# Performance work log

Hardware: AMD Instinct MI355X
Metric: run time of the kernel (lower is better)

The kernel has to match this reference:

```python
import jax, jax.numpy as jnp
import numpy as np

ALPHA = 0.2  # LeakyReLU negative slope


def setup_inputs() -> dict:
    key = jax.random.key(0)
    k1, k2, k3 = jax.random.split(key, 3)
    B, N, D_in, D_out = 16, 2048, 128, 128
    x = jax.random.normal(k1, (B, N, D_in), dtype=jnp.float32)
    # xavier-uniform-ish scale for params
    W = jax.random.normal(k2, (D_in, D_out), dtype=jnp.float32) * (1.414 / np.sqrt(D_in + D_out))
    a = jax.random.normal(k3, (2 * D_out, 1), dtype=jnp.float32) * (1.414 / np.sqrt(2 * D_out + 1))
    return {"x": x, "W": W, "a": a}


def reference(x, W, a):
    # h: (B, N, D)
    h = jnp.matmul(x, W)
    D = h.shape[-1]
    # a = [a1; a2]; e[b,i,j] = leakyrelu(a1 . h_i + a2 . h_j)
    a1 = a[:D, 0]   # (D,)
    a2 = a[D:, 0]   # (D,)
    s1 = jnp.einsum('bnd,d->bn', h, a1)  # (B, N) source term
    s2 = jnp.einsum('bnd,d->bn', h, a2)  # (B, N) target term
    e = jax.nn.leaky_relu(s1[:, :, None] + s2[:, None, :], negative_slope=ALPHA)  # (B, N, N)
    attention = jax.nn.softmax(e, axis=2)
    h_prime = jnp.matmul(attention, h)  # (B, N, D)
    return jax.nn.relu(h_prime)  # concat=True -> relu
```

## Files before the change

### kernel.cpp

```cpp
#include <hip/hip_runtime.h>
#include <hip/hip_bf16.h>
#include <cstddef>

#define GAT_B 16
#define GAT_N 2048
#define GAT_D 128
#define GAT_ROWS (GAT_B * GAT_N)
#define CH 128
#define CL 16
#define GAT_ALPHA 0.2f

typedef __attribute__((ext_vector_type(8))) short short8v;
typedef __attribute__((ext_vector_type(4))) float f32x4;

__device__ __forceinline__ void cvt_hilo(float x, unsigned short& hi, unsigned short& lo) {
  union { float f; unsigned u; } a;
  a.f = x;
  hi = (unsigned short)(a.u >> 16);
  union { unsigned u; float f; } b;
  b.u = (unsigned)hi << 16;
  union { float f; unsigned u; } c;
  c.f = x - b.f;
  lo = (unsigned short)(c.u >> 16);
}

__global__ __launch_bounds__(256) void k0_wfrag(const float* __restrict__ W,
                                                unsigned short* __restrict__ WfH,
                                                unsigned short* __restrict__ WfL) {
  const int t = blockIdx.x * 256 + threadIdx.x;
  const int n = t & 127, g = (t >> 7) & 3, ks = t >> 9;
  short8v vh, vl;
#pragma unroll
  for (int j = 0; j < 8; ++j) {
    const int k = ks * 32 + g * 8 + j;
    unsigned short hi, lo;
    cvt_hilo(W[k * 128 + n], hi, lo);
    vh[j] = (short)hi;
    vl[j] = (short)lo;
  }
  *(short8v*)&WfH[t * 8] = vh;
  *(short8v*)&WfL[t * 8] = vl;
}

__global__ __launch_bounds__(256) void k1_gemm(const float* __restrict__ x,
                                               const unsigned short* __restrict__ WfHg,
                                               const unsigned short* __restrict__ WfLg,
                                               const float* __restrict__ aa,
                                               float* __restrict__ h,
                                               float* __restrict__ s1part,
                                               float* __restrict__ s2part) {
  __shared__ unsigned short xH[64 * 128];
  __shared__ unsigned short xL[64 * 128];
  const int tid = threadIdx.x;
  const int row0 = blockIdx.x * 64;

#pragma unroll
  for (int p = 0; p < 8; ++p) {
    const int row = p * 8 + (tid >> 5);
    const int f4 = tid & 31;
    const float4 v = ((const float4*)(x + (size_t)(row0 + row) * GAT_D))[f4];
    unsigned short h0, h1, h2, h3, l0, l1, l2, l3;
    cvt_hilo(v.x, h0, l0);
    cvt_hilo(v.y, h1, l1);
    cvt_hilo(v.z, h2, l2);
    cvt_hilo(v.w, h3, l3);
    const int slot = (f4 >> 1) ^ (row & 7);
    const int base = row * 128 + slot * 8 + (f4 & 1) * 4;
    *(ushort4*)&xH[base] = make_ushort4(h0, h1, h2, h3);
    *(ushort4*)&xL[base] = make_ushort4(l0, l1, l2, l3);
  }

  const int w = tid >> 6, l = tid & 63;
  const int wc0 = w * 32;
  const int g = l >> 4, c16 = l & 15;

  short8v bh[4][2], bl[4][2];
#pragma unroll
  for (int ks = 0; ks < 4; ++ks)
#pragma unroll
    for (int nt = 0; nt < 2; ++nt) {
      const int bi = ((ks * 4 + g) * 128 + wc0 + nt * 16 + c16) * 8;
      bh[ks][nt] = *(const short8v*)&WfHg[bi];
      bl[ks][nt] = *(const short8v*)&WfLg[bi];
    }

  __syncthreads();

  f32x4 acc[4][2];
#pragma unroll
  for (int mt = 0; mt < 4; ++mt)
#pragma unroll
    for (int nt = 0; nt < 2; ++nt) acc[mt][nt] = (f32x4)(0.f);

#pragma unroll
  for (int ks = 0; ks < 4; ++ks) {
    short8v ah[4], al[4];
#pragma unroll
    for (int mt = 0; mt < 4; ++mt) {
      const int row = mt * 16 + c16;
      const int ai = row * 128 + (((ks * 4 + g) ^ (row & 7)) * 8);
      ah[mt] = *(const short8v*)&xH[ai];
      al[mt] = *(const short8v*)&xL[ai];
    }
#pragma unroll
    for (int mt = 0; mt < 4; ++mt) {
#pragma unroll
      for (int nt = 0; nt < 2; ++nt) {
        acc[mt][nt] = __builtin_amdgcn_mfma_f32_16x16x32_bf16(ah[mt], bh[ks][nt], acc[mt][nt], 0, 0, 0);
        acc[mt][nt] = __builtin_amdgcn_mfma_f32_16x16x32_bf16(al[mt], bh[ks][nt], acc[mt][nt], 0, 0, 0);
        acc[mt][nt] = __builtin_amdgcn_mfma_f32_16x16x32_bf16(ah[mt], bl[ks][nt], acc[mt][nt], 0, 0, 0);
      }
    }
  }

#pragma unroll
  for (int mt = 0; mt < 4; ++mt)
#pragma unroll
    for (int nt = 0; nt < 2; ++nt)
#pragma unroll
      for (int j = 0; j < 4; ++j)
        h[(size_t)(row0 + mt * 16 + g * 4 + j) * GAT_D + wc0 + nt * 16 + c16] =
            acc[mt][nt][j];

  float a1v[2], a2v[2];
#pragma unroll
  for (int nt = 0; nt < 2; ++nt) {
    a1v[nt] = aa[wc0 + nt * 16 + c16];
    a2v[nt] = aa[128 + wc0 + nt * 16 + c16];
  }
#pragma unroll
  for (int mt = 0; mt < 4; ++mt) {
#pragma unroll
    for (int j = 0; j < 4; ++j) {
      float t1 = acc[mt][0][j] * a1v[0] + acc[mt][1][j] * a1v[1];
      float t2 = acc[mt][0][j] * a2v[0] + acc[mt][1][j] * a2v[1];
#pragma unroll
      for (int off = 1; off < 16; off <<= 1) {
        t1 += __shfl_xor(t1, off);
        t2 += __shfl_xor(t2, off);
      }
      if (c16 == 0) {
        const int row = row0 + mt * 16 + g * 4 + j;
        s1part[w * GAT_ROWS + row] = t1;
        s2part[w * GAT_ROWS + row] = t2;
      }
    }
  }
}

__global__ __launch_bounds__(1024) void k2_sort(const float* __restrict__ s1part,
                                                const float* __restrict__ s2part,
                                                float* __restrict__ s2s,
                                                int* __restrict__ idxs,
                                                float* __restrict__ s1s,
                                                int* __restrict__ rids,
                                                float* __restrict__ wA,
                                                float* __restrict__ wP,
                                                float* __restrict__ preDenA,
                                                float* __restrict__ sufDenP) {
  __shared__ float v[2048];
  __shared__ int id[2048];
  __shared__ float wtotA[16];
  __shared__ float wtotP[16];
  const int tid = threadIdx.x;
  const int b = blockIdx.x >> 1;
  const int half = blockIdx.x & 1;
  const int i0 = tid, i1 = tid + 1024;
  const float* src = (half == 0) ? s2part : s1part;
  {
    const int r0 = b * GAT_N + i0, r1 = b * GAT_N + i1;
    float v0 = src[r0] + src[GAT_ROWS + r0] + src[2 * GAT_ROWS + r0] + src[3 * GAT_ROWS + r0];
    float v1 = src[r1] + src[GAT_ROWS + r1] + src[2 * GAT_ROWS + r1] + src[3 * GAT_ROWS + r1];
    if (half == 1) {
      v0 = -v0;
      v1 = -v1;
    }
    v[i0] = v0;
    v[i1] = v1;
  }
  id[i0] = i0;
  id[i1] = i1;
  for (int k = 2; k <= 2048; k <<= 1) {
    for (int j = k >> 1; j > 0; j >>= 1) {
      __syncthreads();
      const int i = ((tid & ~(j - 1)) << 1) | (tid & (j - 1));
      const int ixj = i | j;
      const bool up = (i & k) == 0;
      const float va = v[i], vb = v[ixj];
      if (up ? (va > vb) : (va < vb)) {
        v[i] = vb;
        v[ixj] = va;
        const int ta = id[i];
        id[i] = id[ixj];
        id[ixj] = ta;
      }
    }
  }
  __syncthreads();
  if (half == 1) {
    s1s[b * GAT_N + i0] = -v[i0];
    s1s[b * GAT_N + i1] = -v[i1];
    rids[b * GAT_N + i0] = id[i0];
    rids[b * GAT_N + i1] = id[i1];
    return;
  }
  s2s[b * GAT_N + i0] = v[i0];
  s2s[b * GAT_N + i1] = v[i1];
  idxs[b * GAT_N + i0] = id[i0];
  idxs[b * GAT_N + i1] = id[i1];

  const int lane = tid & 63, w = tid >> 6;
  const float aL = __expf(GAT_ALPHA * v[2 * tid]);
  const float aR = __expf(GAT_ALPHA * v[2 * tid + 1]);
  const float pL = __expf(v[2047 - 2 * tid]);
  const float pR = __expf(v[2046 - 2 * tid]);
  wA[b * GAT_N + 2 * tid] = aL;
  wA[b * GAT_N + 2 * tid + 1] = aR;
  wP[b * GAT_N + 2047 - 2 * tid] = pL;
  wP[b * GAT_N + 2046 - 2 * tid] = pR;
  float sA = aL + aR, sP = pL + pR;
#pragma unroll
  for (int off = 1; off < 64; off <<= 1) {
    const float tA = __shfl_up(sA, off);
    const float tP = __shfl_up(sP, off);
    if (lane >= off) {
      sA += tA;
      sP += tP;
    }
  }
  if (lane == 63) {
    wtotA[w] = sA;
    wtotP[w] = sP;
  }
  __syncthreads();
  float offA = 0.f, offP = 0.f;
  for (int ww = 0; ww < w; ++ww) {
    offA += wtotA[ww];
    offP += wtotP[ww];
  }
  const float inclA = offA + sA;
  const float inclP = offP + sP;
  preDenA[b * GAT_N + 2 * tid] = inclA - aR;
  preDenA[b * GAT_N + 2 * tid + 1] = inclA;
  sufDenP[b * GAT_N + 2047 - 2 * tid] = inclP - pR;
  sufDenP[b * GAT_N + 2046 - 2 * tid] = inclP;
}

__global__ __launch_bounds__(128) void k3_permute(const float* __restrict__ h,
                                                  const int* __restrict__ idxs,
                                                  const float* __restrict__ wA,
                                                  const float* __restrict__ wP,
                                                  float* __restrict__ hs,
                                                  float* __restrict__ partA,
                                                  float* __restrict__ partP) {
  const int b = blockIdx.x >> 7, c = blockIdx.x & (CH - 1);
  const int d = threadIdx.x;
  const int q0 = c * CL;
  const int* idxb = idxs + b * GAT_N;
  const float* hb = h + (size_t)b * GAT_N * GAT_D;
  float accA = 0.f, accP = 0.f;
#pragma unroll
  for (int qq = 0; qq < CL; ++qq) {
    const int q = q0 + qq;
    const int j = idxb[q];
    const float hv = hb[(size_t)j * GAT_D + d];
    hs[((size_t)b * GAT_N + q) * GAT_D + d] = hv;
    accA = fmaf(wA[b * GAT_N + q], hv, accA);
    accP = fmaf(wP[b * GAT_N + q], hv, accP);
  }
  partA[(b * CH + c) * GAT_D + d] = accA;
  partP[(b * CH + c) * GAT_D + d] = accP;
}

__global__ __launch_bounds__(1024) void k3b_prep(const float* __restrict__ s1s,
                                                 const float* __restrict__ s2s,
                                                 const float* __restrict__ preDenA,
                                                 const float* __restrict__ sufDenP,
                                                 const float* __restrict__ partA,
                                                 const float* __restrict__ partP,
                                                 float* __restrict__ baseA,
                                                 float* __restrict__ baseP,
                                                 int* __restrict__ pArr,
                                                 float* __restrict__ c1,
                                                 float* __restrict__ c2) {
  __shared__ float totA[8][128];
  __shared__ float totP[8][128];
  __shared__ float sh[2048];
  const int b = blockIdx.x >> 1;
  const int role = blockIdx.x & 1;
  const int t = threadIdx.x;
  if (role == 0) {
    const int d = t & 127, g = t >> 7;
    const float* pA = partA + (size_t)(b * CH + g * 16) * GAT_D + d;
    const float* pP = partP + (size_t)(b * CH + g * 16) * GAT_D + d;
    float la[16], lp[16];
    float sA = 0.f, sP = 0.f;
#pragma unroll
    for (int i = 0; i < 16; ++i) {
      la[i] = pA[i * GAT_D];
      sA += la[i];
      lp[i] = pP[i * GAT_D];
      sP += lp[i];
    }
    totA[g][d] = sA;
    totP[g][d] = sP;
    __syncthreads();
    float offA = 0.f, offP = 0.f;
    for (int gg = 0; gg < g; ++gg) offA += totA[gg][d];
    for (int gg = g + 1; gg < 8; ++gg) offP += totP[gg][d];
    float run = offA;
#pragma unroll
    for (int i = 0; i < 16; ++i) {
      baseA[(size_t)(b * (CH + 1) + g * 16 + i) * GAT_D + d] = run;
      run += la[i];
    }
    if (g == 7) baseA[(size_t)(b * (CH + 1) + CH) * GAT_D + d] = run;
    run = offP;
#pragma unroll
    for (int i = 15; i >= 0; --i) {
      baseP[(size_t)(b * CH + g * 16 + i) * GAT_D + d] = run;
      run += lp[i];
    }
  } else {
    sh[t] = s2s[b * GAT_N + t];
    sh[t + 1024] = s2s[b * GAT_N + t + 1024];
    __syncthreads();
#pragma unroll
    for (int rr = 0; rr < 2; ++rr) {
      const int j = t + rr * 1024;
      const float s1v = s1s[b * GAT_N + j];
      const float tt = -s1v;
      int lo = 0, hi = GAT_N;
      while (lo < hi) {
        const int mid = (lo + hi) >> 1;
        if (sh[mid] < tt)
          lo = mid + 1;
        else
          hi = mid;
      }
      const float e1 = __expf(s1v), e2 = __expf(GAT_ALPHA * s1v);
      float den = 0.f;
      if (lo < GAT_N) den += e1 * sufDenP[b * GAT_N + lo];
      if (lo > 0) den += e2 * preDenA[b * GAT_N + lo - 1];
      const float inv = 1.f / den;
      pArr[b * GAT_N + j] = lo;
      c1[b * GAT_N + j] = e1 * inv;
      c2[b * GAT_N + j] = e2 * inv;
    }
  }
}

__global__ __launch_bounds__(256) void k5_out(const float* __restrict__ hs,
                                              const float* __restrict__ wA,
                                              const float* __restrict__ wP,
                                              const float* __restrict__ baseA,
                                              const float* __restrict__ baseP,
                                              const int* __restrict__ pArr,
                                              const float* __restrict__ c1,
                                              const float* __restrict__ c2,
                                              const int* __restrict__ rids,
                                              float* __restrict__ out) {
  const int wave = threadIdx.x >> 6, lane = threadIdx.x & 63;
  const int j = blockIdx.x * 4 + wave;
  const int b = j >> 11;
  const int jr = b * GAT_N + (j & 2047);
  const int p = pArr[jr];
  const float cc1 = c1[jr], cc2 = c2[jr];
  const int rid = rids[jr];
  const float2* hs2 = (const float2*)(hs + (size_t)b * GAT_N * GAT_D);
  const float* wAb = wA + b * GAT_N;
  const float* wPb = wP + b * GAT_N;

  const int cA = p >> 4;
  float2 accA = ((const float2*)(baseA + (size_t)(b * (CH + 1) + cA) * GAT_D))[lane];
  for (int q = cA * CL; q < p; ++q) {
    const float w = wAb[q];
    const float2 hv = hs2[(size_t)q * 64 + lane];
    accA.x = fmaf(w, hv.x, accA.x);
    accA.y = fmaf(w, hv.y, accA.y);
  }

  const int pP = p < GAT_N ? p : GAT_N - 1;
  const int cP = pP >> 4;
  float2 accP = ((const float2*)(baseP + (size_t)(b * CH + cP) * GAT_D))[lane];
  const int qend = cP * CL + CL;
  for (int q = p; q < qend; ++q) {
    const float w = wPb[q];
    const float2 hv = hs2[(size_t)q * 64 + lane];
    accP.x = fmaf(w, hv.x, accP.x);
    accP.y = fmaf(w, hv.y, accP.y);
  }

  const float vx = cc2 * accA.x + cc1 * accP.x;
  const float vy = cc2 * accA.y + cc1 * accP.y;
  ((float2*)out)[(size_t)(b * GAT_N + rid) * 64 + lane] =
      make_float2(fmaxf(vx, 0.f), fmaxf(vy, 0.f));
}

extern "C" void kernel_launch(void* const* d_in, const int* in_sizes, int n_in,
                              void* d_out, int out_size, void* d_ws, size_t ws_size,
                              hipStream_t stream) {
  (void)in_sizes;
  (void)n_in;
  (void)out_size;
  (void)ws_size;
  const float* x = (const float*)d_in[0];
  const float* W = (const float*)d_in[1];
  const float* a = (const float*)d_in[2];
  float* out = (float*)d_out;
  float* wsf = (float*)d_ws;

  const size_t HN = (size_t)GAT_ROWS * GAT_D;
  size_t o = 0;
  float* s1part = wsf + o;   o += 4 * GAT_ROWS;
  float* s2part = wsf + o;   o += 4 * GAT_ROWS;
  float* s2s = wsf + o;      o += GAT_ROWS;
  int* idxs = (int*)(wsf + o); o += GAT_ROWS;
  float* s1s = wsf + o;      o += GAT_ROWS;
  int* rids = (int*)(wsf + o); o += GAT_ROWS;
  float* preDenA = wsf + o;  o += GAT_ROWS;
  float* sufDenP = wsf + o;  o += GAT_ROWS;
  float* wAr = wsf + o;      o += GAT_ROWS;
  float* wPr = wsf + o;      o += GAT_ROWS;
  int* pArr = (int*)(wsf + o); o += GAT_ROWS;
  float* c1 = wsf + o;       o += GAT_ROWS;
  float* c2 = wsf + o;       o += GAT_ROWS;
  float* partA = wsf + o;    o += (size_t)GAT_B * CH * GAT_D;
  float* partP = wsf + o;    o += (size_t)GAT_B * CH * GAT_D;
  float* baseA = wsf + o;    o += (size_t)GAT_B * (CH + 1) * GAT_D;
  float* baseP = wsf + o;    o += (size_t)GAT_B * CH * GAT_D;
  unsigned short* WfH = (unsigned short*)(wsf + o); o += 8192;
  unsigned short* WfL = (unsigned short*)(wsf + o); o += 8192;
  float* h = wsf + o;        o += HN;
  float* hs = wsf + o;       o += HN;

  k0_wfrag<<<8, 256, 0, stream>>>(W, WfH, WfL);
  k1_gemm<<<512, 256, 0, stream>>>(x, WfH, WfL, a, h, s1part, s2part);
  k2_sort<<<2 * GAT_B, 1024, 0, stream>>>(s1part, s2part, s2s, idxs, s1s, rids, wAr, wPr,
                                          preDenA, sufDenP);
  k3_permute<<<GAT_B * CH, 128, 0, stream>>>(h, idxs, wAr, wPr, hs, partA, partP);
  k3b_prep<<<2 * GAT_B, 1024, 0, stream>>>(s1s, s2s, preDenA, sufDenP, partA, partP,
                                           baseA, baseP, pArr, c1, c2);
  k5_out<<<GAT_ROWS / 4, 256, 0, stream>>>(hs, wAr, wPr, baseA, baseP, pArr, c1, c2,
                                           rids, out);
}
```

Before: 82.05 us.

## Replace bitonic sort with parallel rank sort and drop permuted h copy

Replaces the 32-block bitonic sort with a 256-block rank-by-counting kernel using packed 64-bit keys, so each element's sorted position comes from comparing against all 2048 keys in shared memory. The prefix sums of the exp weights move into k3b_prep's shared memory instead of global arrays. The materialized permuted copy hs is removed, and k3 and k5 now gather h through idxs. Chunk size is halved (CL 8, CH 256) to shorten the per-row tail loops. This trades the sort's many barrier phases for O(N) comparisons per element and indirect gathers in the output kernel.

```diff
diff --git a/kernel.cpp b/kernel.cpp
--- a/kernel.cpp
+++ b/kernel.cpp
@@ -6,8 +6,8 @@
 #define GAT_N 2048
 #define GAT_D 128
 #define GAT_ROWS (GAT_B * GAT_N)
-#define CH 128
-#define CL 16
+#define CH 256
+#define CL 8
 #define GAT_ALPHA 0.2f
 
 typedef __attribute__((ext_vector_type(8))) short short8v;
@@ -148,112 +148,59 @@
   }
 }
 
-__global__ __launch_bounds__(1024) void k2_sort(const float* __restrict__ s1part,
+__global__ __launch_bounds__(256) void k2a_rank(const float* __restrict__ s1part,
                                                 const float* __restrict__ s2part,
                                                 float* __restrict__ s2s,
                                                 int* __restrict__ idxs,
                                                 float* __restrict__ s1s,
                                                 int* __restrict__ rids,
                                                 float* __restrict__ wA,
-                                                float* __restrict__ wP,
-                                                float* __restrict__ preDenA,
-                                                float* __restrict__ sufDenP) {
-  __shared__ float v[2048];
-  __shared__ int id[2048];
-  __shared__ float wtotA[16];
-  __shared__ float wtotP[16];
-  const int tid = threadIdx.x;
-  const int b = blockIdx.x >> 1;
-  const int half = blockIdx.x & 1;
-  const int i0 = tid, i1 = tid + 1024;
-  const float* src = (half == 0) ? s2part : s1part;
-  {
-    const int r0 = b * GAT_N + i0, r1 = b * GAT_N + i1;
-    float v0 = src[r0] + src[GAT_ROWS + r0] + src[2 * GAT_ROWS + r0] + src[3 * GAT_ROWS + r0];
-    float v1 = src[r1] + src[GAT_ROWS + r1] + src[2 * GAT_ROWS + r1] + src[3 * GAT_ROWS + r1];
-    if (half == 1) {
-      v0 = -v0;
-      v1 = -v1;
-    }
-    v[i0] = v0;
-    v[i1] = v1;
-  }
-  id[i0] = i0;
-  id[i1] = i1;
-  for (int k = 2; k <= 2048; k <<= 1) {
-    for (int j = k >> 1; j > 0; j >>= 1) {
-      __syncthreads();
-      const int i = ((tid & ~(j - 1)) << 1) | (tid & (j - 1));
-      const int ixj = i | j;
-      const bool up = (i & k) == 0;
-      const float va = v[i], vb = v[ixj];
-      if (up ? (va > vb) : (va < vb)) {
-        v[i] = vb;
-        v[ixj] = va;
-        const int ta = id[i];
-        id[i] = id[ixj];
-        id[ixj] = ta;
-      }
-    }
+                                                float* __restrict__ wP) {
+  __shared__ unsigned long long keys[2048];
+  const int blk = blockIdx.x;
+  const int b = blk >> 4;
+  const int key = (blk >> 3) & 1;
+  const int chunk = blk & 7;
+  const int t = threadIdx.x;
+  const float* src = key ? s1part : s2part;
+#pragma unroll
+  for (int ii = 0; ii < 8; ++ii) {
+    const int i = t + ii * 256;
+    const int r = b * GAT_N + i;
+    float v = src[r] + src[GAT_ROWS + r] + src[2 * GAT_ROWS + r] + src[3 * GAT_ROWS + r];
+    if (key) v = -v;
+    unsigned u = __float_as_uint(v);
+    u = (u & 0x80000000u) ? ~u : (u | 0x80000000u);
+    keys[i] = ((unsigned long long)u << 11) | (unsigned)i;
   }
   __syncthreads();
-  if (half == 1) {
-    s1s[b * GAT_N + i0] = -v[i0];
-    s1s[b * GAT_N + i1] = -v[i1];
-    rids[b * GAT_N + i0] = id[i0];
-    rids[b * GAT_N + i1] = id[i1];
-    return;
-  }
-  s2s[b * GAT_N + i0] = v[i0];
-  s2s[b * GAT_N + i1] = v[i1];
-  idxs[b * GAT_N + i0] = id[i0];
-  idxs[b * GAT_N + i1] = id[i1];
-
-  const int lane = tid & 63, w = tid >> 6;
-  const float aL = __expf(GAT_ALPHA * v[2 * tid]);
-  const float aR = __expf(GAT_ALPHA * v[2 * tid + 1]);
-  const float pL = __expf(v[2047 - 2 * tid]);
-  const float pR = __expf(v[2046 - 2 * tid]);
-  wA[b * GAT_N + 2 * tid] = aL;
-  wA[b * GAT_N + 2 * tid + 1] = aR;
-  wP[b * GAT_N + 2047 - 2 * tid] = pL;
-  wP[b * GAT_N + 2046 - 2 * tid] = pR;
-  float sA = aL + aR, sP = pL + pR;
-#pragma unroll
-  for (int off = 1; off < 64; off <<= 1) {
-    const float tA = __shfl_up(sA, off);
-    const float tP = __shfl_up(sP, off);
-    if (lane >= off) {
-      sA += tA;
-      sP += tP;
-    }
-  }
-  if (lane == 63) {
-    wtotA[w] = sA;
-    wtotP[w] = sP;
-  }
-  __syncthreads();
-  float offA = 0.f, offP = 0.f;
-  for (int ww = 0; ww < w; ++ww) {
-    offA += wtotA[ww];
-    offP += wtotP[ww];
-  }
-  const float inclA = offA + sA;
-  const float inclP = offP + sP;
-  preDenA[b * GAT_N + 2 * tid] = inclA - aR;
-  preDenA[b * GAT_N + 2 * tid + 1] = inclA;
-  sufDenP[b * GAT_N + 2047 - 2 * tid] = inclP - pR;
-  sufDenP[b * GAT_N + 2046 - 2 * tid] = inclP;
-}
-
-__global__ __launch_bounds__(128) void k3_permute(const float* __restrict__ h,
+  const int e = chunk * 256 + t;
+  const unsigned long long myk = keys[e];
+  int rank = 0;
+#pragma unroll 8
+  for (int j = 0; j < 2048; ++j) rank += (keys[j] < myk) ? 1 : 0;
+  const unsigned s = (unsigned)(myk >> 11);
+  const unsigned u = (s & 0x80000000u) ? (s ^ 0x80000000u) : ~s;
+  const float v = __uint_as_float(u);
+  const int o = b * GAT_N + rank;
+  if (key == 0) {
+    s2s[o] = v;
+    idxs[o] = e;
+    wA[o] = __expf(GAT_ALPHA * v);
+    wP[o] = __expf(v);
+  } else {
+    s1s[o] = -v;
+    rids[o] = e;
+  }
+}
+
+__global__ __launch_bounds__(128) void k3_partial(const float* __restrict__ h,
                                                   const int* __restrict__ idxs,
                                                   const float* __restrict__ wA,
                                                   const float* __restrict__ wP,
-                                                  float* __restrict__ hs,
                                                   float* __restrict__ partA,
                                                   float* __restrict__ partP) {
-  const int b = blockIdx.x >> 7, c = blockIdx.x & (CH - 1);
+  const int b = blockIdx.x >> 8, c = blockIdx.x & (CH - 1);
   const int d = threadIdx.x;
   const int q0 = c * CL;
   const int* idxb = idxs + b * GAT_N;
@@ -262,9 +209,7 @@
 #pragma unroll
   for (int qq = 0; qq < CL; ++qq) {
     const int q = q0 + qq;
-    const int j = idxb[q];
-    const float hv = hb[(size_t)j * GAT_D + d];
-    hs[((size_t)b * GAT_N + q) * GAT_D + d] = hv;
+    const float hv = hb[(size_t)idxb[q] * GAT_D + d];
     accA = fmaf(wA[b * GAT_N + q], hv, accA);
     accP = fmaf(wP[b * GAT_N + q], hv, accP);
   }
@@ -274,8 +219,8 @@
 
 __global__ __launch_bounds__(1024) void k3b_prep(const float* __restrict__ s1s,
                                                  const float* __restrict__ s2s,
-                                                 const float* __restrict__ preDenA,
-                                                 const float* __restrict__ sufDenP,
+                                                 const float* __restrict__ wA,
+                                                 const float* __restrict__ wP,
                                                  const float* __restrict__ partA,
                                                  const float* __restrict__ partP,
                                                  float* __restrict__ baseA,
@@ -286,21 +231,22 @@
   __shared__ float totA[8][128];
   __shared__ float totP[8][128];
   __shared__ float sh[2048];
+  __shared__ float denA[2048];
+  __shared__ float denP[2048];
+  __shared__ float wtotA[16];
+  __shared__ float wtotP[16];
   const int b = blockIdx.x >> 1;
   const int role = blockIdx.x & 1;
   const int t = threadIdx.x;
   if (role == 0) {
     const int d = t & 127, g = t >> 7;
-    const float* pA = partA + (size_t)(b * CH + g * 16) * GAT_D + d;
-    const float* pP = partP + (size_t)(b * CH + g * 16) * GAT_D + d;
-    float la[16], lp[16];
+    const float* pA = partA + (size_t)(b * CH + g * 32) * GAT_D + d;
+    const float* pP = partP + (size_t)(b * CH + g * 32) * GAT_D + d;
     float sA = 0.f, sP = 0.f;
-#pragma unroll
-    for (int i = 0; i < 16; ++i) {
-      la[i] = pA[i * GAT_D];
-      sA += la[i];
-      lp[i] = pP[i * GAT_D];
-      sP += lp[i];
+#pragma unroll 8
+    for (int i = 0; i < 32; ++i) {
+      sA += pA[i * GAT_D];
+      sP += pP[i * GAT_D];
     }
     totA[g][d] = sA;
     totP[g][d] = sP;
@@ -309,21 +255,52 @@
     for (int gg = 0; gg < g; ++gg) offA += totA[gg][d];
     for (int gg = g + 1; gg < 8; ++gg) offP += totP[gg][d];
     float run = offA;
-#pragma unroll
-    for (int i = 0; i < 16; ++i) {
-      baseA[(size_t)(b * (CH + 1) + g * 16 + i) * GAT_D + d] = run;
-      run += la[i];
+#pragma unroll 8
+    for (int i = 0; i < 32; ++i) {
+      baseA[(size_t)(b * (CH + 1) + g * 32 + i) * GAT_D + d] = run;
+      run += pA[i * GAT_D];
     }
     if (g == 7) baseA[(size_t)(b * (CH + 1) + CH) * GAT_D + d] = run;
     run = offP;
-#pragma unroll
-    for (int i = 15; i >= 0; --i) {
-      baseP[(size_t)(b * CH + g * 16 + i) * GAT_D + d] = run;
-      run += lp[i];
+#pragma unroll 8
+    for (int i = 31; i >= 0; --i) {
+      baseP[(size_t)(b * CH + g * 32 + i) * GAT_D + d] = run;
+      run += pP[i * GAT_D];
     }
   } else {
     sh[t] = s2s[b * GAT_N + t];
     sh[t + 1024] = s2s[b * GAT_N + t + 1024];
+    const int lane = t & 63, w = t >> 6;
+    const float aL = wA[b * GAT_N + 2 * t];
+    const float aR = wA[b * GAT_N + 2 * t + 1];
+    const float pL = wP[b * GAT_N + 2047 - 2 * t];
+    const float pR = wP[b * GAT_N + 2046 - 2 * t];
+    float sA = aL + aR, sP = pL + pR;
+#pragma unroll
+    for (int off = 1; off < 64; off <<= 1) {
+      const float tA = __shfl_up(sA, off);
+      const float tP = __shfl_up(sP, off);
+      if (lane >= off) {
+        sA += tA;
+        sP += tP;
+      }
+    }
+    if (lane == 63) {
+      wtotA[w] = sA;
+      wtotP[w] = sP;
+    }
+    __syncthreads();
+    float offA = 0.f, offP = 0.f;
+    for (int ww = 0; ww < w; ++ww) {
+      offA += wtotA[ww];
+      offP += wtotP[ww];
+    }
+    const float inclA = offA + sA;
+    const float inclP = offP + sP;
+    denA[2 * t] = inclA - aR;
+    denA[2 * t + 1] = inclA;
+    denP[2047 - 2 * t] = inclP - pR;
+    denP[2046 - 2 * t] = inclP;
     __syncthreads();
 #pragma unroll
     for (int rr = 0; rr < 2; ++rr) {
@@ -340,8 +317,8 @@
       }
       const float e1 = __expf(s1v), e2 = __expf(GAT_ALPHA * s1v);
       float den = 0.f;
-      if (lo < GAT_N) den += e1 * sufDenP[b * GAT_N + lo];
-      if (lo > 0) den += e2 * preDenA[b * GAT_N + lo - 1];
+      if (lo < GAT_N) den += e1 * denP[lo];
+      if (lo > 0) den += e2 * denA[lo - 1];
       const float inv = 1.f / den;
       pArr[b * GAT_N + j] = lo;
       c1[b * GAT_N + j] = e1 * inv;
@@ -350,7 +327,8 @@
   }
 }
 
-__global__ __launch_bounds__(256) void k5_out(const float* __restrict__ hs,
+__global__ __launch_bounds__(256) void k5_out(const float* __restrict__ h,
+                                              const int* __restrict__ idxs,
                                               const float* __restrict__ wA,
                                               const float* __restrict__ wP,
                                               const float* __restrict__ baseA,
@@ -367,26 +345,27 @@
   const int p = pArr[jr];
   const float cc1 = c1[jr], cc2 = c2[jr];
   const int rid = rids[jr];
-  const float2* hs2 = (const float2*)(hs + (size_t)b * GAT_N * GAT_D);
+  const float* hb = h + (size_t)b * GAT_N * GAT_D;
+  const int* idxb = idxs + b * GAT_N;
   const float* wAb = wA + b * GAT_N;
   const float* wPb = wP + b * GAT_N;
 
-  const int cA = p >> 4;
+  const int cA = p >> 3;
   float2 accA = ((const float2*)(baseA + (size_t)(b * (CH + 1) + cA) * GAT_D))[lane];
   for (int q = cA * CL; q < p; ++q) {
     const float w = wAb[q];
-    const float2 hv = hs2[(size_t)q * 64 + lane];
+    const float2 hv = ((const float2*)(hb + (size_t)idxb[q] * GAT_D))[lane];
     accA.x = fmaf(w, hv.x, accA.x);
     accA.y = fmaf(w, hv.y, accA.y);
   }
 
   const int pP = p < GAT_N ? p : GAT_N - 1;
-  const int cP = pP >> 4;
+  const int cP = pP >> 3;
   float2 accP = ((const float2*)(baseP + (size_t)(b * CH + cP) * GAT_D))[lane];
   const int qend = cP * CL + CL;
   for (int q = p; q < qend; ++q) {
     const float w = wPb[q];
-    const float2 hv = hs2[(size_t)q * 64 + lane];
+    const float2 hv = ((const float2*)(hb + (size_t)idxb[q] * GAT_D))[lane];
     accP.x = fmaf(w, hv.x, accP.x);
     accP.y = fmaf(w, hv.y, accP.y);
   }
@@ -418,8 +397,6 @@
   int* idxs = (int*)(wsf + o); o += GAT_ROWS;
   float* s1s = wsf + o;      o += GAT_ROWS;
   int* rids = (int*)(wsf + o); o += GAT_ROWS;
-  float* preDenA = wsf + o;  o += GAT_ROWS;
-  float* sufDenP = wsf + o;  o += GAT_ROWS;
   float* wAr = wsf + o;      o += GAT_ROWS;
   float* wPr = wsf + o;      o += GAT_ROWS;
   int* pArr = (int*)(wsf + o); o += GAT_ROWS;
@@ -432,15 +409,13 @@
   unsigned short* WfH = (unsigned short*)(wsf + o); o += 8192;
   unsigned short* WfL = (unsigned short*)(wsf + o); o += 8192;
   float* h = wsf + o;        o += HN;
-  float* hs = wsf + o;       o += HN;
 
   k0_wfrag<<<8, 256, 0, stream>>>(W, WfH, WfL);
   k1_gemm<<<512, 256, 0, stream>>>(x, WfH, WfL, a, h, s1part, s2part);
-  k2_sort<<<2 * GAT_B, 1024, 0, stream>>>(s1part, s2part, s2s, idxs, s1s, rids, wAr, wPr,
-                                          preDenA, sufDenP);
-  k3_permute<<<GAT_B * CH, 128, 0, stream>>>(h, idxs, wAr, wPr, hs, partA, partP);
-  k3b_prep<<<2 * GAT_B, 1024, 0, stream>>>(s1s, s2s, preDenA, sufDenP, partA, partP,
+  k2a_rank<<<256, 256, 0, stream>>>(s1part, s2part, s2s, idxs, s1s, rids, wAr, wPr);
+  k3_partial<<<GAT_B * CH, 128, 0, stream>>>(h, idxs, wAr, wPr, partA, partP);
+  k3b_prep<<<2 * GAT_B, 1024, 0, stream>>>(s1s, s2s, wAr, wPr, partA, partP,
                                            baseA, baseP, pArr, c1, c2);
-  k5_out<<<GAT_ROWS / 4, 256, 0, stream>>>(hs, wAr, wPr, baseA, baseP, pArr, c1, c2,
-                                           rids, out);
-}
+  k5_out<<<GAT_ROWS / 4, 256, 0, stream>>>(h, idxs, wAr, wPr, baseA, baseP, pArr,
+                                           c1, c2, rids, out);
+}
```

Measured after the change: 94.31 us. 1.15x slower.
